# Kernel optimization log

Measured on AMD Instinct MI355X. Metric: run time of the kernel, lower is better.

## Reference

```python
import jax, jax.numpy as jnp
import numpy as np

N, K, D, OUT = 50000, 16, 128, 128


def setup_inputs() -> dict:
    key = jax.random.key(0)
    ks = jax.random.split(key, 10)
    s = 0.05
    return {
        'feat': jax.random.normal(ks[0], (N, D), dtype=jnp.float32),
        'neigh_idx': jax.random.randint(ks[1], (N, K), 0, N, dtype=jnp.int32),
        'W_ih': jax.random.normal(ks[2], (3 * D, D), dtype=jnp.float32) * s,
        'W_hh': jax.random.normal(ks[3], (3 * D, D), dtype=jnp.float32) * s,
        'b_ih': jax.random.normal(ks[4], (3 * D,), dtype=jnp.float32) * s,
        'b_hh': jax.random.normal(ks[5], (3 * D,), dtype=jnp.float32) * s,
        'W_self': jax.random.normal(ks[6], (OUT, D), dtype=jnp.float32) * s,
        'W_neigh': jax.random.normal(ks[7], (OUT, D), dtype=jnp.float32) * s,
        'alpha': jnp.full((OUT,), 0.25, dtype=jnp.float32),  # PReLU default init
    }


def _gru_final_hidden(m, W_ih, W_hh, b_ih, b_hh):
    # m: [N, K, D] mailbox; returns final hidden state hn: [N, D]
    # torch.nn.GRU cell: r,z,n gate ordering in weight layout
    def step(h, x):
        gi = x @ W_ih.T + b_ih            # [N, 3D]
        gh = h @ W_hh.T + b_hh            # [N, 3D]
        gi_r, gi_z, gi_n = jnp.split(gi, 3, axis=-1)
        gh_r, gh_z, gh_n = jnp.split(gh, 3, axis=-1)
        r = jax.nn.sigmoid(gi_r + gh_r)
        z = jax.nn.sigmoid(gi_z + gh_z)
        n = jnp.tanh(gi_n + r * gh_n)
        h_new = (1.0 - z) * n + z * h
        return h_new, None

    h0 = jnp.zeros((m.shape[0], m.shape[2]), dtype=m.dtype)
    xs = jnp.swapaxes(m, 0, 1)            # [K, N, D] scan over sequence
    hn, _ = jax.lax.scan(step, h0, xs)
    return hn


def reference(feat, neigh_idx, W_ih, W_hh, b_ih, b_hh, W_self, W_neigh, alpha):
    # gather neighbor mailbox (copy_u): [N, K, D]
    m = jnp.take(feat, neigh_idx, axis=0)
    neigh = _gru_final_hidden(m, W_ih, W_hh, b_ih, b_hh)  # [N, D]
    rst = feat @ W_self.T + neigh @ W_neigh.T             # [N, OUT]
    # per-channel PReLU
    return jnp.where(rst >= 0, rst, alpha * rst)
```

## Files before the change

kernel.cpp:

```cpp
#include <hip/hip_runtime.h>
#include <stdint.h>

typedef __attribute__((ext_vector_type(8))) short short8;
typedef __attribute__((ext_vector_type(4))) float float4v;
typedef unsigned short u16;
typedef unsigned int u32;

#define D_DIM 128
#define K_NEI 16
#define G_ROW32 192

__device__ __forceinline__ float bf2f(u16 v) {
  union { u32 u; float f; } c; c.u = ((u32)v) << 16; return c.f;
}
__device__ __forceinline__ u16 f2bf(float f) {
  union { float f; u32 u; } c; c.f = f;
  u32 r = c.u + 0x7FFFu + ((c.u >> 16) & 1u);
  return (u16)(r >> 16);
}
__device__ __forceinline__ float lo_f(u32 v) {
  union { u32 u; float f; } c; c.u = v << 16; return c.f;
}
__device__ __forceinline__ float hi_f(u32 v) {
  union { u32 u; float f; } c; c.u = v & 0xFFFF0000u; return c.f;
}
__device__ __forceinline__ float fsigmoid(float x) {
  return __builtin_amdgcn_rcpf(1.0f + __expf(-x));
}
__device__ __forceinline__ float ftanh_(float x) {
  return 1.0f - 2.0f * __builtin_amdgcn_rcpf(1.0f + __expf(2.0f * x));
}
__device__ __forceinline__ float4v mfma16(short8 a, short8 b, float4v c) {
  return __builtin_amdgcn_mfma_f32_16x16x32_bf16(a, b, c, 0, 0, 0);
}
__device__ __forceinline__ float4v splat4(float v) { float4v r = {v, v, v, v}; return r; }

__device__ __forceinline__ short8 ldrow8(const u16* pb, const float* pf, bool isbf, long off) {
  if (isbf) return *(const short8*)(pb + off);
  const float* p = pf + off;
  short8 r;
#pragma unroll
  for (int i = 0; i < 8; ++i) r[i] = (short)f2bf(p[i]);
  return r;
}

__global__ __launch_bounds__(256, 2)
void gi_gemm(const void* feat_raw, const void* wih_raw, const void* bih_raw,
             const u32* alpha_w, u32* G, int n_nodes) {
  const bool isbf = (alpha_w[0] == 0x3E803E80u);
  const u16* featb = (const u16*)feat_raw; const float* featf = (const float*)feat_raw;
  const u16* wihb  = (const u16*)wih_raw;  const float* wihf  = (const float*)wih_raw;
  const u16* bihb  = (const u16*)bih_raw;  const float* bihf  = (const float*)bih_raw;

  const int tid = threadIdx.x, w = tid >> 6, lane = tid & 63;
  const int quad = lane >> 4, l15 = lane & 15;
  const int nb = blockIdx.x * 64;
  const int cw = w * 32;

  short8 fih[6][4];
#pragma unroll
  for (int g = 0; g < 3; ++g)
#pragma unroll
    for (int s = 0; s < 2; ++s) {
      int row = g * 128 + cw + s * 16 + l15;
#pragma unroll
      for (int kt = 0; kt < 4; ++kt)
        fih[g * 2 + s][kt] = ldrow8(wihb, wihf, isbf, (long)row * 128 + kt * 32 + quad * 8);
    }
  float bi[6];
#pragma unroll
  for (int g = 0; g < 3; ++g)
#pragma unroll
    for (int s = 0; s < 2; ++s) {
      int col = g * 128 + cw + s * 16 + l15;
      bi[g * 2 + s] = isbf ? bf2f(bihb[col]) : bihf[col];
    }

  float4v acc[4][6];
#pragma unroll
  for (int m = 0; m < 4; ++m)
#pragma unroll
    for (int t = 0; t < 6; ++t) acc[m][t] = splat4(0.0f);

  short8 abuf[2][4];
  {
    int node = nb + l15; if (node > n_nodes - 1) node = n_nodes - 1;
#pragma unroll
    for (int kt = 0; kt < 4; ++kt)
      abuf[0][kt] = ldrow8(featb, featf, isbf, (long)node * 128 + kt * 32 + quad * 8);
  }
#pragma unroll
  for (int m = 0; m < 4; ++m) {
    if (m < 3) {
      int node = nb + (m + 1) * 16 + l15; if (node > n_nodes - 1) node = n_nodes - 1;
#pragma unroll
      for (int kt = 0; kt < 4; ++kt)
        abuf[(m + 1) & 1][kt] = ldrow8(featb, featf, isbf, (long)node * 128 + kt * 32 + quad * 8);
    }
#pragma unroll
    for (int kt = 0; kt < 4; ++kt)
#pragma unroll
      for (int t = 0; t < 6; ++t) acc[m][t] = mfma16(abuf[m & 1][kt], fih[t][kt], acc[m][t]);
  }

#pragma unroll
  for (int m = 0; m < 4; ++m)
#pragma unroll
    for (int j = 0; j < 4; ++j) {
      int node = nb + m * 16 + quad * 4 + j;
      if (node < n_nodes) {
        u32* p = G + (long)node * G_ROW32 + w * 48 + l15;
#pragma unroll
        for (int g = 0; g < 3; ++g) {
          u32 vlo = f2bf(acc[m][g * 2 + 0][j] + bi[g * 2 + 0]);
          u32 vhi = f2bf(acc[m][g * 2 + 1][j] + bi[g * 2 + 1]);
          p[g * 16] = vlo | (vhi << 16);
        }
      }
    }
}

__device__ __forceinline__ void prefetch_g(u32 (*buf)[4][3], const u32* G,
                                           const int (*sidx)[32], int kk,
                                           int w, int quad, int l15) {
#pragma unroll
  for (int m = 0; m < 2; ++m)
#pragma unroll
    for (int j = 0; j < 4; ++j) {
      int gidx = sidx[kk][m * 16 + quad * 4 + j];
      const u32* gp = G + (long)gidx * G_ROW32 + w * 48 + l15;
      buf[m][j][0] = gp[0];
      buf[m][j][1] = gp[16];
      buf[m][j][2] = gp[32];
    }
}

__global__ __launch_bounds__(256, 2)
void gru_fused(const void* feat_raw, const int* nidx,
               const void* whh_raw, const void* bhh_raw,
               const void* wself_raw, const void* wneigh_raw,
               const void* alpha_raw, void* out_raw,
               const u32* G, int n_nodes) {
  const bool isbf = (((const u32*)alpha_raw)[0] == 0x3E803E80u);
  const u16* featb   = (const u16*)feat_raw;   const float* featf   = (const float*)feat_raw;
  const u16* whhb    = (const u16*)whh_raw;    const float* whhf    = (const float*)whh_raw;
  const u16* bhhb    = (const u16*)bhh_raw;    const float* bhhf    = (const float*)bhh_raw;
  const u16* wselfb  = (const u16*)wself_raw;  const float* wselff  = (const float*)wself_raw;
  const u16* wneighb = (const u16*)wneigh_raw; const float* wneighf = (const float*)wneigh_raw;

  const int tid  = threadIdx.x;
  const int w    = tid >> 6;
  const int lane = tid & 63;
  const int quad = lane >> 4;
  const int l15  = lane & 15;
  const int nb   = blockIdx.x * 32;
  const int cw   = w * 32;

  __shared__ __align__(16) u16 hbuf[2][32 * 136];
  __shared__ int sidx[K_NEI][32];

  for (int t = tid; t < 32 * K_NEI; t += 256) {
    int n = t >> 4, kk = t & 15;
    int node = nb + n;
    sidx[kk][n] = (node < n_nodes) ? nidx[(long)nb * K_NEI + t]
                                   : nidx[(long)(n_nodes - 1) * K_NEI + kk];
  }

  float bhh_rz[4], bhh_n[2];
#pragma unroll
  for (int s = 0; s < 2; ++s) {
    int rr = cw + s * 16 + l15;
    if (isbf) {
      bhh_rz[s]     = bf2f(bhhb[rr]);
      bhh_rz[2 + s] = bf2f(bhhb[128 + rr]);
      bhh_n[s]      = bf2f(bhhb[256 + rr]);
    } else {
      bhh_rz[s]     = bhhf[rr];
      bhh_rz[2 + s] = bhhf[128 + rr];
      bhh_n[s]      = bhhf[256 + rr];
    }
  }

  short8 fhh[6][4];
#pragma unroll
  for (int g = 0; g < 3; ++g)
#pragma unroll
    for (int s = 0; s < 2; ++s) {
      int row = g * 128 + cw + s * 16 + l15;
#pragma unroll
      for (int kt = 0; kt < 4; ++kt)
        fhh[g * 2 + s][kt] = ldrow8(whhb, whhf, isbf, (long)row * 128 + kt * 32 + quad * 8);
    }

#pragma unroll
  for (int m = 0; m < 2; ++m)
#pragma unroll
    for (int s = 0; s < 2; ++s)
#pragma unroll
      for (int j = 0; j < 4; ++j)
        hbuf[0][(m * 16 + quad * 4 + j) * 136 + cw + s * 16 + l15] = 0;

  float hreg[2][2][4] = {};
  __syncthreads();

  u32 gbuf[2][2][4][3];
  prefetch_g(gbuf[0], G, sidx, 0, w, quad, l15);

#pragma unroll 2
  for (int k = 0; k < K_NEI; ++k) {
    if (k + 1 < K_NEI) prefetch_g(gbuf[(k + 1) & 1], G, sidx, k + 1, w, quad, l15);

    float4v arz[2][4], aghn[2][2];
#pragma unroll
    for (int m = 0; m < 2; ++m) {
#pragma unroll
      for (int t = 0; t < 4; ++t) arz[m][t] = splat4(bhh_rz[t]);
#pragma unroll
      for (int s = 0; s < 2; ++s) aghn[m][s] = splat4(bhh_n[s]);
    }

    const u16* hr = hbuf[k & 1];
#pragma unroll
    for (int m = 0; m < 2; ++m) {
      short8 ah[4];
#pragma unroll
      for (int kt = 0; kt < 4; ++kt)
        ah[kt] = *(const short8*)(hr + (m * 16 + l15) * 136 + kt * 32 + quad * 8);
#pragma unroll
      for (int kt = 0; kt < 4; ++kt) {
        arz[m][0]  = mfma16(ah[kt], fhh[0][kt], arz[m][0]);
        arz[m][1]  = mfma16(ah[kt], fhh[1][kt], arz[m][1]);
        arz[m][2]  = mfma16(ah[kt], fhh[2][kt], arz[m][2]);
        arz[m][3]  = mfma16(ah[kt], fhh[3][kt], arz[m][3]);
        aghn[m][0] = mfma16(ah[kt], fhh[4][kt], aghn[m][0]);
        aghn[m][1] = mfma16(ah[kt], fhh[5][kt], aghn[m][1]);
      }
    }

#pragma unroll
    for (int m = 0; m < 2; ++m)
#pragma unroll
      for (int j = 0; j < 4; ++j) {
        u32 rp = gbuf[k & 1][m][j][0];
        u32 zp = gbuf[k & 1][m][j][1];
        u32 np = gbuf[k & 1][m][j][2];
        {
          float rv = fsigmoid(lo_f(rp) + arz[m][0][j]);
          float zv = fsigmoid(lo_f(zp) + arz[m][2][j]);
          float nv = ftanh_(lo_f(np) + rv * aghn[m][0][j]);
          hreg[m][0][j] = (1.0f - zv) * nv + zv * hreg[m][0][j];
        }
        {
          float rv = fsigmoid(hi_f(rp) + arz[m][1][j]);
          float zv = fsigmoid(hi_f(zp) + arz[m][3][j]);
          float nv = ftanh_(hi_f(np) + rv * aghn[m][1][j]);
          hreg[m][1][j] = (1.0f - zv) * nv + zv * hreg[m][1][j];
        }
      }

    if (k + 1 < K_NEI) {
      u16* hw2 = hbuf[(k + 1) & 1];
#pragma unroll
      for (int m = 0; m < 2; ++m)
#pragma unroll
        for (int s = 0; s < 2; ++s)
#pragma unroll
          for (int j = 0; j < 4; ++j)
            hw2[(m * 16 + quad * 4 + j) * 136 + cw + s * 16 + l15] = f2bf(hreg[m][s][j]);
      __syncthreads();
    }
  }

  u16* hw = hbuf[0];
#pragma unroll
  for (int m = 0; m < 2; ++m)
#pragma unroll
    for (int s = 0; s < 2; ++s)
#pragma unroll
      for (int j = 0; j < 4; ++j)
        hw[(m * 16 + quad * 4 + j) * 136 + cw + s * 16 + l15] = f2bf(hreg[m][s][j]);
  __syncthreads();

  short8 af[2][4], ahf[2][4];
#pragma unroll
  for (int m = 0; m < 2; ++m) {
    int node = nb + m * 16 + l15;
    if (node > n_nodes - 1) node = n_nodes - 1;
#pragma unroll
    for (int kt = 0; kt < 4; ++kt) {
      af[m][kt]  = ldrow8(featb, featf, isbf, (long)node * 128 + kt * 32 + quad * 8);
      ahf[m][kt] = *(const short8*)(hbuf[0] + (m * 16 + l15) * 136 + kt * 32 + quad * 8);
    }
  }
  float4v ao[2][2];
#pragma unroll
  for (int m = 0; m < 2; ++m)
#pragma unroll
    for (int s = 0; s < 2; ++s) ao[m][s] = splat4(0.0f);
#pragma unroll
  for (int s = 0; s < 2; ++s) {
    int row = cw + s * 16 + l15;
#pragma unroll
    for (int kt = 0; kt < 4; ++kt) {
      short8 bs = ldrow8(wselfb,  wselff,  isbf, (long)row * 128 + kt * 32 + quad * 8);
      short8 bn = ldrow8(wneighb, wneighf, isbf, (long)row * 128 + kt * 32 + quad * 8);
#pragma unroll
      for (int m = 0; m < 2; ++m) {
        ao[m][s] = mfma16(af[m][kt],  bs, ao[m][s]);
        ao[m][s] = mfma16(ahf[m][kt], bn, ao[m][s]);
      }
    }
  }
  float av[2];
#pragma unroll
  for (int s = 0; s < 2; ++s) {
    int c = cw + s * 16 + l15;
    av[s] = isbf ? bf2f(((const u16*)alpha_raw)[c]) : ((const float*)alpha_raw)[c];
  }
#pragma unroll
  for (int m = 0; m < 2; ++m)
#pragma unroll
    for (int s = 0; s < 2; ++s)
#pragma unroll
      for (int j = 0; j < 4; ++j) {
        int node = nb + m * 16 + quad * 4 + j;
        if (node < n_nodes) {
          float v = ao[m][s][j];
          v = (v >= 0.0f) ? v : av[s] * v;
          long off = (long)node * 128 + cw + s * 16 + l15;
          if (isbf) ((u16*)out_raw)[off] = f2bf(v);
          else      ((float*)out_raw)[off] = v;
        }
      }
}

extern "C" void kernel_launch(void* const* d_in, const int* in_sizes, int n_in,
                              void* d_out, int out_size, void* d_ws, size_t ws_size,
                              hipStream_t stream) {
  (void)n_in; (void)out_size; (void)ws_size;
  const int n_nodes = in_sizes[0] / D_DIM;
  u32* G = (u32*)d_ws;
  const int gblocks = (n_nodes + 63) / 64;
  hipLaunchKernelGGL(gi_gemm, dim3(gblocks), dim3(256), 0, stream,
                     d_in[0], d_in[2], d_in[4], (const u32*)d_in[8], G, n_nodes);
  const int nblocks = (n_nodes + 31) / 32;
  hipLaunchKernelGGL(gru_fused, dim3(nblocks), dim3(256), 0, stream,
                     d_in[0], (const int*)d_in[1], d_in[3], d_in[5],
                     d_in[6], d_in[7], d_in[8], d_out, (const u32*)G, n_nodes);
}
```

Measured before the change: 329.3 us.

## Split GRU recurrence across 8 waves per block with 16 columns each

The fused GRU kernel moves from 256 to 512 threads per block. Each wave now owns 16 hidden columns instead of 32, which halves the per-thread W_hh fragments, accumulators and gathered gate buffers, and the launch bounds are raised to allow more resident waves. The G prefetch for the next step is moved after the gate math and interleaved per m-tile, and the barrier is replaced with an explicit lgkmcnt wait plus s_barrier. The aim is lower register pressure and more latency hiding. The cost is twice the LDS reads of h per block and more waves contending at each barrier.

```diff
diff --git a/kernel.cpp b/kernel.cpp
--- a/kernel.cpp
+++ b/kernel.cpp
@@ -23,6 +23,9 @@
 }
 __device__ __forceinline__ float hi_f(u32 v) {
   union { u32 u; float f; } c; c.u = v & 0xFFFF0000u; return c.f;
+}
+__device__ __forceinline__ float half_f(u32 v, u32 shl) {
+  union { u32 u; float f; } c; c.u = (v << shl) & 0xFFFF0000u; return c.f;
 }
 __device__ __forceinline__ float fsigmoid(float x) {
   return __builtin_amdgcn_rcpf(1.0f + __expf(-x));
@@ -120,22 +123,7 @@
     }
 }
 
-__device__ __forceinline__ void prefetch_g(u32 (*buf)[4][3], const u32* G,
-                                           const int (*sidx)[32], int kk,
-                                           int w, int quad, int l15) {
-#pragma unroll
-  for (int m = 0; m < 2; ++m)
-#pragma unroll
-    for (int j = 0; j < 4; ++j) {
-      int gidx = sidx[kk][m * 16 + quad * 4 + j];
-      const u32* gp = G + (long)gidx * G_ROW32 + w * 48 + l15;
-      buf[m][j][0] = gp[0];
-      buf[m][j][1] = gp[16];
-      buf[m][j][2] = gp[32];
-    }
-}
-
-__global__ __launch_bounds__(256, 2)
+__global__ __launch_bounds__(512, 4)
 void gru_fused(const void* feat_raw, const int* nidx,
                const void* whh_raw, const void* bhh_raw,
                const void* wself_raw, const void* wneigh_raw,
@@ -149,136 +137,121 @@
   const u16* wneighb = (const u16*)wneigh_raw; const float* wneighf = (const float*)wneigh_raw;
 
   const int tid  = threadIdx.x;
-  const int w    = tid >> 6;
+  const int w8   = tid >> 6;
   const int lane = tid & 63;
   const int quad = lane >> 4;
   const int l15  = lane & 15;
   const int nb   = blockIdx.x * 32;
-  const int cw   = w * 32;
+  const int w4   = w8 >> 1;
+  const u32 shl  = (w8 & 1) ? 0u : 16u;
+  const int cw   = w8 * 16;
 
   __shared__ __align__(16) u16 hbuf[2][32 * 136];
   __shared__ int sidx[K_NEI][32];
 
-  for (int t = tid; t < 32 * K_NEI; t += 256) {
+  {
+    int t = tid;
     int n = t >> 4, kk = t & 15;
     int node = nb + n;
     sidx[kk][n] = (node < n_nodes) ? nidx[(long)nb * K_NEI + t]
                                    : nidx[(long)(n_nodes - 1) * K_NEI + kk];
   }
 
-  float bhh_rz[4], bhh_n[2];
-#pragma unroll
-  for (int s = 0; s < 2; ++s) {
-    int rr = cw + s * 16 + l15;
+  float bhh_r, bhh_z, bhh_n;
+  {
+    int c = cw + l15;
     if (isbf) {
-      bhh_rz[s]     = bf2f(bhhb[rr]);
-      bhh_rz[2 + s] = bf2f(bhhb[128 + rr]);
-      bhh_n[s]      = bf2f(bhhb[256 + rr]);
+      bhh_r = bf2f(bhhb[c]); bhh_z = bf2f(bhhb[128 + c]); bhh_n = bf2f(bhhb[256 + c]);
     } else {
-      bhh_rz[s]     = bhhf[rr];
-      bhh_rz[2 + s] = bhhf[128 + rr];
-      bhh_n[s]      = bhhf[256 + rr];
-    }
-  }
-
-  short8 fhh[6][4];
-#pragma unroll
-  for (int g = 0; g < 3; ++g)
-#pragma unroll
-    for (int s = 0; s < 2; ++s) {
-      int row = g * 128 + cw + s * 16 + l15;
-#pragma unroll
-      for (int kt = 0; kt < 4; ++kt)
-        fhh[g * 2 + s][kt] = ldrow8(whhb, whhf, isbf, (long)row * 128 + kt * 32 + quad * 8);
-    }
+      bhh_r = bhhf[c];       bhh_z = bhhf[128 + c];       bhh_n = bhhf[256 + c];
+    }
+  }
+
+  short8 fhh[3][4];
+#pragma unroll
+  for (int g = 0; g < 3; ++g) {
+    int row = g * 128 + cw + l15;
+#pragma unroll
+    for (int kt = 0; kt < 4; ++kt)
+      fhh[g][kt] = ldrow8(whhb, whhf, isbf, (long)row * 128 + kt * 32 + quad * 8);
+  }
 
 #pragma unroll
   for (int m = 0; m < 2; ++m)
 #pragma unroll
-    for (int s = 0; s < 2; ++s)
-#pragma unroll
-      for (int j = 0; j < 4; ++j)
-        hbuf[0][(m * 16 + quad * 4 + j) * 136 + cw + s * 16 + l15] = 0;
-
-  float hreg[2][2][4] = {};
+    for (int j = 0; j < 4; ++j)
+      hbuf[0][(m * 16 + quad * 4 + j) * 136 + cw + l15] = 0;
+
+  float hreg[2][4] = {};
   __syncthreads();
 
-  u32 gbuf[2][2][4][3];
-  prefetch_g(gbuf[0], G, sidx, 0, w, quad, l15);
+  u32 gbuf[2][4][3];
+#pragma unroll
+  for (int m = 0; m < 2; ++m)
+#pragma unroll
+    for (int j = 0; j < 4; ++j) {
+      int gidx = sidx[0][m * 16 + quad * 4 + j];
+      const u32* gp = G + (long)gidx * G_ROW32 + w4 * 48 + l15;
+      gbuf[m][j][0] = gp[0];
+      gbuf[m][j][1] = gp[16];
+      gbuf[m][j][2] = gp[32];
+    }
 
 #pragma unroll 2
   for (int k = 0; k < K_NEI; ++k) {
-    if (k + 1 < K_NEI) prefetch_g(gbuf[(k + 1) & 1], G, sidx, k + 1, w, quad, l15);
-
-    float4v arz[2][4], aghn[2][2];
+    const u16* hr = hbuf[k & 1];
+    u16* hw = hbuf[(k + 1) & 1];
+
 #pragma unroll
     for (int m = 0; m < 2; ++m) {
-#pragma unroll
-      for (int t = 0; t < 4; ++t) arz[m][t] = splat4(bhh_rz[t]);
-#pragma unroll
-      for (int s = 0; s < 2; ++s) aghn[m][s] = splat4(bhh_n[s]);
-    }
-
-    const u16* hr = hbuf[k & 1];
-#pragma unroll
-    for (int m = 0; m < 2; ++m) {
-      short8 ah[4];
-#pragma unroll
-      for (int kt = 0; kt < 4; ++kt)
-        ah[kt] = *(const short8*)(hr + (m * 16 + l15) * 136 + kt * 32 + quad * 8);
+      float4v ar = splat4(bhh_r), az = splat4(bhh_z), an = splat4(bhh_n);
 #pragma unroll
       for (int kt = 0; kt < 4; ++kt) {
-        arz[m][0]  = mfma16(ah[kt], fhh[0][kt], arz[m][0]);
-        arz[m][1]  = mfma16(ah[kt], fhh[1][kt], arz[m][1]);
-        arz[m][2]  = mfma16(ah[kt], fhh[2][kt], arz[m][2]);
-        arz[m][3]  = mfma16(ah[kt], fhh[3][kt], arz[m][3]);
-        aghn[m][0] = mfma16(ah[kt], fhh[4][kt], aghn[m][0]);
-        aghn[m][1] = mfma16(ah[kt], fhh[5][kt], aghn[m][1]);
-      }
-    }
-
+        short8 a = *(const short8*)(hr + (m * 16 + l15) * 136 + kt * 32 + quad * 8);
+        ar = mfma16(a, fhh[0][kt], ar);
+        az = mfma16(a, fhh[1][kt], az);
+        an = mfma16(a, fhh[2][kt], an);
+      }
+
+#pragma unroll
+      for (int j = 0; j < 4; ++j) {
+        u32 rp = gbuf[m][j][0];
+        u32 zp = gbuf[m][j][1];
+        u32 np = gbuf[m][j][2];
+        float rv = fsigmoid(half_f(rp, shl) + ar[j]);
+        float zv = fsigmoid(half_f(zp, shl) + az[j]);
+        float nv = ftanh_(half_f(np, shl) + rv * an[j]);
+        hreg[m][j] = (1.0f - zv) * nv + zv * hreg[m][j];
+      }
+
+      if (k + 1 < K_NEI) {
+#pragma unroll
+        for (int j = 0; j < 4; ++j) {
+          int gidx = sidx[k + 1][m * 16 + quad * 4 + j];
+          const u32* gp = G + (long)gidx * G_ROW32 + w4 * 48 + l15;
+          gbuf[m][j][0] = gp[0];
+          gbuf[m][j][1] = gp[16];
+          gbuf[m][j][2] = gp[32];
+        }
+#pragma unroll
+        for (int j = 0; j < 4; ++j)
+          hw[(m * 16 + quad * 4 + j) * 136 + cw + l15] = f2bf(hreg[m][j]);
+      }
+    }
+
+    if (k + 1 < K_NEI) {
+      asm volatile("s_waitcnt lgkmcnt(0)\n\ts_barrier" ::: "memory");
+    }
+  }
+
+  {
+    u16* hw = hbuf[0];
 #pragma unroll
     for (int m = 0; m < 2; ++m)
 #pragma unroll
-      for (int j = 0; j < 4; ++j) {
-        u32 rp = gbuf[k & 1][m][j][0];
-        u32 zp = gbuf[k & 1][m][j][1];
-        u32 np = gbuf[k & 1][m][j][2];
-        {
-          float rv = fsigmoid(lo_f(rp) + arz[m][0][j]);
-          float zv = fsigmoid(lo_f(zp) + arz[m][2][j]);
-          float nv = ftanh_(lo_f(np) + rv * aghn[m][0][j]);
-          hreg[m][0][j] = (1.0f - zv) * nv + zv * hreg[m][0][j];
-        }
-        {
-          float rv = fsigmoid(hi_f(rp) + arz[m][1][j]);
-          float zv = fsigmoid(hi_f(zp) + arz[m][3][j]);
-          float nv = ftanh_(hi_f(np) + rv * aghn[m][1][j]);
-          hreg[m][1][j] = (1.0f - zv) * nv + zv * hreg[m][1][j];
-        }
-      }
-
-    if (k + 1 < K_NEI) {
-      u16* hw2 = hbuf[(k + 1) & 1];
-#pragma unroll
-      for (int m = 0; m < 2; ++m)
-#pragma unroll
-        for (int s = 0; s < 2; ++s)
-#pragma unroll
-          for (int j = 0; j < 4; ++j)
-            hw2[(m * 16 + quad * 4 + j) * 136 + cw + s * 16 + l15] = f2bf(hreg[m][s][j]);
-      __syncthreads();
-    }
-  }
-
-  u16* hw = hbuf[0];
-#pragma unroll
-  for (int m = 0; m < 2; ++m)
-#pragma unroll
-    for (int s = 0; s < 2; ++s)
-#pragma unroll
       for (int j = 0; j < 4; ++j)
-        hw[(m * 16 + quad * 4 + j) * 136 + cw + s * 16 + l15] = f2bf(hreg[m][s][j]);
+        hw[(m * 16 + quad * 4 + j) * 136 + cw + l15] = f2bf(hreg[m][j]);
+  }
   __syncthreads();
 
   short8 af[2][4], ahf[2][4];
@@ -292,46 +265,39 @@
       ahf[m][kt] = *(const short8*)(hbuf[0] + (m * 16 + l15) * 136 + kt * 32 + quad * 8);
     }
   }
-  float4v ao[2][2];
-#pragma unroll
-  for (int m = 0; m < 2; ++m)
-#pragma unroll
-    for (int s = 0; s < 2; ++s) ao[m][s] = splat4(0.0f);
-#pragma unroll
-  for (int s = 0; s < 2; ++s) {
-    int row = cw + s * 16 + l15;
+  float4v ao[2];
+  ao[0] = splat4(0.0f); ao[1] = splat4(0.0f);
+  {
+    int row = cw + l15;
 #pragma unroll
     for (int kt = 0; kt < 4; ++kt) {
       short8 bs = ldrow8(wselfb,  wselff,  isbf, (long)row * 128 + kt * 32 + quad * 8);
       short8 bn = ldrow8(wneighb, wneighf, isbf, (long)row * 128 + kt * 32 + quad * 8);
 #pragma unroll
       for (int m = 0; m < 2; ++m) {
-        ao[m][s] = mfma16(af[m][kt],  bs, ao[m][s]);
-        ao[m][s] = mfma16(ahf[m][kt], bn, ao[m][s]);
-      }
-    }
-  }
-  float av[2];
-#pragma unroll
-  for (int s = 0; s < 2; ++s) {
-    int c = cw + s * 16 + l15;
-    av[s] = isbf ? bf2f(((const u16*)alpha_raw)[c]) : ((const float*)alpha_raw)[c];
+        ao[m] = mfma16(af[m][kt],  bs, ao[m]);
+        ao[m] = mfma16(ahf[m][kt], bn, ao[m]);
+      }
+    }
+  }
+  float av;
+  {
+    int c = cw + l15;
+    av = isbf ? bf2f(((const u16*)alpha_raw)[c]) : ((const float*)alpha_raw)[c];
   }
 #pragma unroll
   for (int m = 0; m < 2; ++m)
 #pragma unroll
-    for (int s = 0; s < 2; ++s)
-#pragma unroll
-      for (int j = 0; j < 4; ++j) {
-        int node = nb + m * 16 + quad * 4 + j;
-        if (node < n_nodes) {
-          float v = ao[m][s][j];
-          v = (v >= 0.0f) ? v : av[s] * v;
-          long off = (long)node * 128 + cw + s * 16 + l15;
-          if (isbf) ((u16*)out_raw)[off] = f2bf(v);
-          else      ((float*)out_raw)[off] = v;
-        }
-      }
+    for (int j = 0; j < 4; ++j) {
+      int node = nb + m * 16 + quad * 4 + j;
+      if (node < n_nodes) {
+        float v = ao[m][j];
+        v = (v >= 0.0f) ? v : av * v;
+        long off = (long)node * 128 + cw + l15;
+        if (isbf) ((u16*)out_raw)[off] = f2bf(v);
+        else      ((float*)out_raw)[off] = v;
+      }
+    }
 }
 
 extern "C" void kernel_launch(void* const* d_in, const int* in_sizes, int n_in,
@@ -344,7 +310,7 @@
   hipLaunchKernelGGL(gi_gemm, dim3(gblocks), dim3(256), 0, stream,
                      d_in[0], d_in[2], d_in[4], (const u32*)d_in[8], G, n_nodes);
   const int nblocks = (n_nodes + 31) / 32;
-  hipLaunchKernelGGL(gru_fused, dim3(nblocks), dim3(256), 0, stream,
+  hipLaunchKernelGGL(gru_fused, dim3(nblocks), dim3(512), 0, stream,
                      d_in[0], (const int*)d_in[1], d_in[3], d_in[5],
                      d_in[6], d_in[7], d_in[8], d_out, (const u32*)G, n_nodes);
 }
```

After: 319.9 us. 1.03x faster.
